# Kernel optimization log

Hardware: AMD Instinct MI355X
Metric: run time of the kernel (lower is better)

## Reference

```python
import jax, jax.numpy as jnp
import numpy as np

NPROTOS = 40      # forced by init_offset_tensor reshape
NCLASS  = 512     # number of child classes
C       = 64      # genetic feature channels (pshape[0])
W       = 40      # genetic sequence width (hard-coded in offset tensor)
B       = 1024    # batch
P       = NPROTOS * NCLASS  # 20480 total prototypes
EPS     = 1e-12   # F.normalize eps


def _build_last_layer_weight():
    # match[j, j // nprotos] = 1, weight = match.T with zeros -> -0.5
    match = np.zeros((P, NCLASS), np.float32)
    match[np.arange(P), np.arange(P) // NPROTOS] = 1.0
    w = match.T.copy()
    w[w == 0] = -0.5
    return jnp.asarray(w)


def _build_offset_tensor():
    # arange2[i, j] = (i - j) % nprotos; nprotos == 40 so arange3 is empty
    i = np.arange(NPROTOS)[:, None]
    j = np.arange(NPROTOS)[None, :]
    ar2 = (i - j) % NPROTOS                                  # (40, 40)
    off = np.tile(ar2.reshape(NPROTOS, 1, 1, NPROTOS), (NCLASS, C, 1, 1))
    return jnp.asarray(off.astype(np.int32))                 # (P, C, 1, W)


def setup_inputs() -> dict:
    key = jax.random.key(0)
    k1, k2 = jax.random.split(key)
    conv_features = jax.random.normal(k1, (B, C, 1, W), dtype=jnp.float32)
    prototype = jax.random.uniform(k2, (P, C, 1, 1), dtype=jnp.float32)  # torch.rand
    return {
        "conv_features": conv_features,
        "prototype": prototype,
        "last_layer_weight": _build_last_layer_weight(),
        "offset_tensor": _build_offset_tensor(),
    }


def _l2norm(x, axis):
    # F.normalize: x / max(||x||_2, eps)
    return x / jnp.maximum(jnp.linalg.norm(x, axis=axis, keepdims=True), EPS)


def reference(conv_features, prototype, last_layer_weight, offset_tensor):
    sqrt_D = 1.0  # sqrt(pshape[1] * pshape[2]) = sqrt(1*1)
    x = _l2norm(conv_features, axis=1) / sqrt_D              # (B, C, 1, W)
    p = _l2norm(prototype, axis=1) / sqrt_D                  # (P, C, 1, 1)
    # pad prototypes to width W, then per-prototype spatial offset gather
    p = jnp.pad(p, ((0, 0), (0, 0), (0, 0), (0, W - 1)))     # (P, C, 1, W)
    p = jnp.take_along_axis(p, offset_tensor, axis=3)        # (P, C, 1, W)
    # conv2d with full-width kernel -> output (B, P, 1, 1); max_pool over 1x1 is identity
    sim = jnp.einsum('bchw,pchw->bp', x, p)                  # (B, P)
    min_distances = -sim                                     # view(-1, nclass*nprotos)
    logits = sim @ last_layer_weight.T                       # (B, NCLASS)
    return (logits, min_distances)
```

## Files before the change

kernel.cpp:

```cpp
#include <hip/hip_runtime.h>
#include <math.h>

#define NB 1024
#define NC 64
#define NW 40
#define NK 512
#define NP 20480
#define EPSF 1e-12f


__global__ __launch_bounds__(256) void knorm_p(const float* __restrict__ proto,
                                               float* __restrict__ pn) {
    int wave = threadIdx.x >> 6;
    int lane = threadIdx.x & 63;
    int p = blockIdx.x * 4 + wave;
    float v = proto[p * 64 + lane];
    float s = v * v;
#pragma unroll
    for (int off = 32; off >= 1; off >>= 1) s += __shfl_xor(s, off);
    float r = 1.0f / fmaxf(sqrtf(s), EPSF);
    int j = p % NW, k = p / NW;
    pn[(j * NK + k) * 64 + lane] = v * r;
}

__global__ __launch_bounds__(256) void knorm_x(const float* __restrict__ x,
                                               float* __restrict__ xn) {
    __shared__ float xs[64 * 41];
    __shared__ float rn[40];
    int b = blockIdx.x;
    const float* xb = x + b * (64 * 40);
    for (int t = threadIdx.x; t < 2560; t += 256) {
        int c = t / 40, w = t % 40;
        xs[c * 41 + w] = xb[t];
    }
    __syncthreads();
    if (threadIdx.x < 40) {
        int w = threadIdx.x;
        float s = 0.f;
#pragma unroll
        for (int c = 0; c < 64; ++c) { float v = xs[c * 41 + w]; s += v * v; }
        rn[w] = 1.0f / fmaxf(sqrtf(s), EPSF);
    }
    __syncthreads();
    for (int t = threadIdx.x; t < 2560; t += 256) {
        int w = t >> 6, c = t & 63;
        xn[(w * NB + b) * 64 + c] = xs[c * 41 + w] * rn[w];
    }
}

__global__ __launch_bounds__(256) void kgemm(const float* __restrict__ xn,
                                             const float* __restrict__ pn,
                                             float* __restrict__ simt) {
    __shared__ float4 Xs[128 * 16];
    __shared__ float4 Ps[128 * 16];
    int b0 = blockIdx.x * 128;
    int k0 = blockIdx.y * 128;
    int j  = blockIdx.z;
    const float4* xg = (const float4*)(xn + (size_t)(j * NB + b0) * 64);
    const float4* pg = (const float4*)(pn + (size_t)(j * NK + k0) * 64);
    for (int g = threadIdx.x; g < 2048; g += 256) {
        int row = g >> 4, c4 = g & 15;
        int idx = (row << 4) + (c4 ^ (row >> 3));
        Xs[idx] = xg[g];
        Ps[idx] = pg[g];
    }
    __syncthreads();
    int tb = threadIdx.x >> 4, tk = threadIdx.x & 15;
    float acc[8][8];
#pragma unroll
    for (int i = 0; i < 8; ++i)
#pragma unroll
        for (int q = 0; q < 8; ++q) acc[i][q] = 0.f;

    for (int c4 = 0; c4 < 16; ++c4) {
        float4 xv[8];
#pragma unroll
        for (int i = 0; i < 8; ++i) {
            int row = tb + 16 * i;
            xv[i] = Xs[(row << 4) + (c4 ^ (row >> 3))];
        }
#pragma unroll
        for (int q = 0; q < 8; ++q) {
            int row = tk * 8 + q;
            float4 pv = Ps[(row << 4) + (c4 ^ tk)];
#pragma unroll
            for (int i = 0; i < 8; ++i)
                acc[i][q] += xv[i].x * pv.x + xv[i].y * pv.y +
                             xv[i].z * pv.z + xv[i].w * pv.w;
        }
    }

#pragma unroll
    for (int i = 0; i < 8; ++i) {
        int b = b0 + tb + 16 * i;
        float4* dst = (float4*)(simt + (size_t)b * NP + j * NK + k0 + tk * 8);
        dst[0] = make_float4(acc[i][0], acc[i][1], acc[i][2], acc[i][3]);
        dst[1] = make_float4(acc[i][4], acc[i][5], acc[i][6], acc[i][7]);
    }
}

__global__ __launch_bounds__(256) void ktrans(const float* __restrict__ simt,
                                              float* __restrict__ out) {
    __shared__ float ld[128][41];
    __shared__ float wred[4];
    int b = blockIdx.x;
    int t = threadIdx.x;
    const float* src = simt + (size_t)b * NP;
    float* md = out + (size_t)NB * NK + (size_t)b * NP;
    float rk[4];
    float my_tot = 0.f;

#pragma unroll
    for (int pass = 0; pass < 4; ++pass) {
        int k0 = pass << 7;
#pragma unroll
        for (int s = 0; s < 5; ++s) {
            int idx = s * 256 + t;
            int jj = idx >> 5, f4 = idx & 31;
            float4 v = *(const float4*)(src + jj * NK + k0 + f4 * 4);
            ld[f4 * 4 + 0][jj] = v.x;
            ld[f4 * 4 + 1][jj] = v.y;
            ld[f4 * 4 + 2][jj] = v.z;
            ld[f4 * 4 + 3][jj] = v.w;
        }
        __syncthreads();
        if (t < 128) {
            float s = 0.f;
#pragma unroll
            for (int jj = 0; jj < 40; ++jj) s += ld[t][jj];
            rk[pass] = s;
            my_tot += s;
        }
#pragma unroll
        for (int s2 = 0; s2 < 5; ++s2) {
            int pl = s2 * 1024 + t * 4;
            int kk = pl / 40;
            int jj = pl - kk * 40;
            float vv[4];
#pragma unroll
            for (int e = 0; e < 4; ++e) {
                vv[e] = -ld[kk][jj];
                if (++jj == 40) { jj = 0; ++kk; }
            }
            *(float4*)(md + k0 * 40 + pl) = make_float4(vv[0], vv[1], vv[2], vv[3]);
        }
        __syncthreads();
    }

    float s = my_tot;
#pragma unroll
    for (int off = 32; off >= 1; off >>= 1) s += __shfl_xor(s, off);
    if ((t & 63) == 0) wred[t >> 6] = s;
    __syncthreads();
    float S = wred[0] + wred[1] + wred[2] + wred[3];
    if (t < 128) {
#pragma unroll
        for (int pass = 0; pass < 4; ++pass)
            out[(size_t)b * NK + (pass << 7) + t] = 1.5f * rk[pass] - 0.5f * S;
    }
}

extern "C" void kernel_launch(void* const* d_in, const int* in_sizes, int n_in,
                              void* d_out, int out_size, void* d_ws, size_t ws_size,
                              hipStream_t stream) {
    (void)in_sizes; (void)n_in; (void)out_size; (void)ws_size;
    const float* conv  = (const float*)d_in[0];
    const float* proto = (const float*)d_in[1];
    float* out = (float*)d_out;
    float* ws = (float*)d_ws;
    float* pn   = ws;
    float* xn   = ws + 1310720;
    float* simt = ws + 3932160;

    knorm_p<<<5120, 256, 0, stream>>>(proto, pn);
    knorm_x<<<1024, 256, 0, stream>>>(conv, xn);
    kgemm<<<dim3(8, 4, 40), 256, 0, stream>>>(xn, pn, simt);
    ktrans<<<1024, 256, 0, stream>>>(simt, out);
}
```

Before: 355.8 us.

## Store normalized inputs and similarity intermediate in fp16, merge norm kernels

Normalized x and prototypes, and the intermediate similarity matrix, are stored as fp16 instead of fp32, halving workspace traffic between the norm, GEMM and transpose kernels. The two normalization kernels are fused into one launch, and the transpose kernel is restructured to process 256 classes per pass with an fp16 shared tile. The cost is reduced precision in min_distances and logits (fp16 rounding of sim), which risks tolerance failures.

```diff
diff --git a/kernel.cpp b/kernel.cpp
--- a/kernel.cpp
+++ b/kernel.cpp
@@ -1,4 +1,5 @@
 #include <hip/hip_runtime.h>
+#include <hip/hip_fp16.h>
 #include <math.h>
 
 #define NB 1024
@@ -9,62 +10,78 @@
 #define EPSF 1e-12f
 
 
-__global__ __launch_bounds__(256) void knorm_p(const float* __restrict__ proto,
-                                               float* __restrict__ pn) {
-    int wave = threadIdx.x >> 6;
-    int lane = threadIdx.x & 63;
-    int p = blockIdx.x * 4 + wave;
-    float v = proto[p * 64 + lane];
-    float s = v * v;
-#pragma unroll
-    for (int off = 32; off >= 1; off >>= 1) s += __shfl_xor(s, off);
-    float r = 1.0f / fmaxf(sqrtf(s), EPSF);
-    int j = p % NW, k = p / NW;
-    pn[(j * NK + k) * 64 + lane] = v * r;
-}
-
-__global__ __launch_bounds__(256) void knorm_x(const float* __restrict__ x,
-                                               float* __restrict__ xn) {
+__global__ __launch_bounds__(256) void knorm(const float* __restrict__ conv,
+                                             const float* __restrict__ proto,
+                                             __half* __restrict__ xnh,
+                                             __half* __restrict__ pnh) {
     __shared__ float xs[64 * 41];
     __shared__ float rn[40];
-    int b = blockIdx.x;
-    const float* xb = x + b * (64 * 40);
-    for (int t = threadIdx.x; t < 2560; t += 256) {
-        int c = t / 40, w = t % 40;
-        xs[c * 41 + w] = xb[t];
-    }
-    __syncthreads();
-    if (threadIdx.x < 40) {
-        int w = threadIdx.x;
-        float s = 0.f;
+    int blk = blockIdx.x;
+    if (blk < NB) {
+        int b = blk;
+        const float* xb = conv + b * (64 * 40);
+        for (int t = threadIdx.x; t < 2560; t += 256) {
+            int c = t / 40, w = t % 40;
+            xs[c * 41 + w] = xb[t];
+        }
+        __syncthreads();
+        if (threadIdx.x < 40) {
+            int w = threadIdx.x;
+            float s = 0.f;
 #pragma unroll
-        for (int c = 0; c < 64; ++c) { float v = xs[c * 41 + w]; s += v * v; }
-        rn[w] = 1.0f / fmaxf(sqrtf(s), EPSF);
-    }
-    __syncthreads();
-    for (int t = threadIdx.x; t < 2560; t += 256) {
-        int w = t >> 6, c = t & 63;
-        xn[(w * NB + b) * 64 + c] = xs[c * 41 + w] * rn[w];
+            for (int c = 0; c < 64; ++c) { float v = xs[c * 41 + w]; s += v * v; }
+            rn[w] = 1.0f / fmaxf(sqrtf(s), EPSF);
+        }
+        __syncthreads();
+        for (int t = threadIdx.x; t < 2560; t += 256) {
+            int w = t >> 6, c = t & 63;
+            xnh[((size_t)w * NB + b) * 64 + c] = __float2half(xs[c * 41 + w] * rn[w]);
+        }
+    } else {
+        int p = (blk - NB) * 4 + (threadIdx.x >> 6);
+        int lane = threadIdx.x & 63;
+        float v = proto[p * 64 + lane];
+        float s = v * v;
+#pragma unroll
+        for (int off = 32; off >= 1; off >>= 1) s += __shfl_xor(s, off);
+        float r = 1.0f / fmaxf(sqrtf(s), EPSF);
+        int j = p % NW, k = p / NW;
+        pnh[((size_t)j * NK + k) * 64 + lane] = __float2half(v * r);
     }
 }
 
-__global__ __launch_bounds__(256) void kgemm(const float* __restrict__ xn,
-                                             const float* __restrict__ pn,
-                                             float* __restrict__ simt) {
+__global__ __launch_bounds__(256, 2) void kgemm(const __half* __restrict__ xnh,
+                                                const __half* __restrict__ pnh,
+                                                __half* __restrict__ simt) {
     __shared__ float4 Xs[128 * 16];
     __shared__ float4 Ps[128 * 16];
     int b0 = blockIdx.x * 128;
     int k0 = blockIdx.y * 128;
     int j  = blockIdx.z;
-    const float4* xg = (const float4*)(xn + (size_t)(j * NB + b0) * 64);
-    const float4* pg = (const float4*)(pn + (size_t)(j * NK + k0) * 64);
-    for (int g = threadIdx.x; g < 2048; g += 256) {
-        int row = g >> 4, c4 = g & 15;
-        int idx = (row << 4) + (c4 ^ (row >> 3));
-        Xs[idx] = xg[g];
-        Ps[idx] = pg[g];
+    const __half* xg = xnh + ((size_t)j * NB + b0) * 64;
+    const __half* pg = pnh + ((size_t)j * NK + k0) * 64;
+
+    for (int g = threadIdx.x; g < 1024; g += 256) {
+        int row = g >> 3, ch = g & 7;
+        uint4 ux = *(const uint4*)(xg + (size_t)row * 64 + ch * 8);
+        uint4 up = *(const uint4*)(pg + (size_t)row * 64 + ch * 8);
+        float2 x01 = __half22float2(*(__half2*)&ux.x);
+        float2 x23 = __half22float2(*(__half2*)&ux.y);
+        float2 x45 = __half22float2(*(__half2*)&ux.z);
+        float2 x67 = __half22float2(*(__half2*)&ux.w);
+        float2 p01 = __half22float2(*(__half2*)&up.x);
+        float2 p23 = __half22float2(*(__half2*)&up.y);
+        float2 p45 = __half22float2(*(__half2*)&up.z);
+        float2 p67 = __half22float2(*(__half2*)&up.w);
+        int xk = row & 7, pk = (row >> 3) & 7;
+        int c4a = ch * 2, c4b = ch * 2 + 1;
+        Xs[(row << 4) + (c4a ^ xk)] = make_float4(x01.x, x01.y, x23.x, x23.y);
+        Xs[(row << 4) + (c4b ^ xk)] = make_float4(x45.x, x45.y, x67.x, x67.y);
+        Ps[(row << 4) + (c4a ^ pk)] = make_float4(p01.x, p01.y, p23.x, p23.y);
+        Ps[(row << 4) + (c4b ^ pk)] = make_float4(p45.x, p45.y, p67.x, p67.y);
     }
     __syncthreads();
+
     int tb = threadIdx.x >> 4, tk = threadIdx.x & 15;
     float acc[8][8];
 #pragma unroll
@@ -77,12 +94,12 @@
 #pragma unroll
         for (int i = 0; i < 8; ++i) {
             int row = tb + 16 * i;
-            xv[i] = Xs[(row << 4) + (c4 ^ (row >> 3))];
+            xv[i] = Xs[(row << 4) + (c4 ^ (row & 7))];
         }
 #pragma unroll
         for (int q = 0; q < 8; ++q) {
             int row = tk * 8 + q;
-            float4 pv = Ps[(row << 4) + (c4 ^ tk)];
+            float4 pv = Ps[(row << 4) + (c4 ^ (tk & 7))];
 #pragma unroll
             for (int i = 0; i < 8; ++i)
                 acc[i][q] += xv[i].x * pv.x + xv[i].y * pv.y +
@@ -93,56 +110,55 @@
 #pragma unroll
     for (int i = 0; i < 8; ++i) {
         int b = b0 + tb + 16 * i;
-        float4* dst = (float4*)(simt + (size_t)b * NP + j * NK + k0 + tk * 8);
-        dst[0] = make_float4(acc[i][0], acc[i][1], acc[i][2], acc[i][3]);
-        dst[1] = make_float4(acc[i][4], acc[i][5], acc[i][6], acc[i][7]);
+        union { __half2 h2[4]; uint4 u; } st;
+        st.h2[0] = __halves2half2(__float2half(acc[i][0]), __float2half(acc[i][1]));
+        st.h2[1] = __halves2half2(__float2half(acc[i][2]), __float2half(acc[i][3]));
+        st.h2[2] = __halves2half2(__float2half(acc[i][4]), __float2half(acc[i][5]));
+        st.h2[3] = __halves2half2(__float2half(acc[i][6]), __float2half(acc[i][7]));
+        *(uint4*)(simt + (size_t)b * NP + j * NK + k0 + tk * 8) = st.u;
     }
 }
 
-__global__ __launch_bounds__(256) void ktrans(const float* __restrict__ simt,
+__global__ __launch_bounds__(256) void ktrans(const __half* __restrict__ simt,
                                               float* __restrict__ out) {
-    __shared__ float ld[128][41];
+    __shared__ __half ldh[40][520];
     __shared__ float wred[4];
     int b = blockIdx.x;
     int t = threadIdx.x;
-    const float* src = simt + (size_t)b * NP;
+    const __half* src = simt + (size_t)b * NP;
     float* md = out + (size_t)NB * NK + (size_t)b * NP;
-    float rk[4];
+    float rk[2];
     float my_tot = 0.f;
 
 #pragma unroll
-    for (int pass = 0; pass < 4; ++pass) {
-        int k0 = pass << 7;
+    for (int kp = 0; kp < 2; ++kp) {
+        int k0 = kp << 8;
 #pragma unroll
-        for (int s = 0; s < 5; ++s) {
-            int idx = s * 256 + t;
-            int jj = idx >> 5, f4 = idx & 31;
-            float4 v = *(const float4*)(src + jj * NK + k0 + f4 * 4);
-            ld[f4 * 4 + 0][jj] = v.x;
-            ld[f4 * 4 + 1][jj] = v.y;
-            ld[f4 * 4 + 2][jj] = v.z;
-            ld[f4 * 4 + 3][jj] = v.w;
+        for (int r = 0; r < 5; ++r) {
+            int idx = r * 256 + t;
+            int j = idx >> 5, ch = idx & 31;
+            uint4 v = *(const uint4*)(src + j * NK + k0 + ch * 8);
+            *(uint4*)(&ldh[j][ch * 8]) = v;
         }
         __syncthreads();
-        if (t < 128) {
+        {
             float s = 0.f;
 #pragma unroll
-            for (int jj = 0; jj < 40; ++jj) s += ld[t][jj];
-            rk[pass] = s;
+            for (int j = 0; j < 40; ++j) s += __half2float(ldh[j][t]);
+            rk[kp] = s;
             my_tot += s;
         }
 #pragma unroll
-        for (int s2 = 0; s2 < 5; ++s2) {
-            int pl = s2 * 1024 + t * 4;
-            int kk = pl / 40;
-            int jj = pl - kk * 40;
-            float vv[4];
+        for (int r = 0; r < 10; ++r) {
+            int pl = (r * 256 + t) * 4;
+            int kk = pl / 40, jj = pl - kk * 40;
+            float w[4];
 #pragma unroll
             for (int e = 0; e < 4; ++e) {
-                vv[e] = -ld[kk][jj];
+                w[e] = -__half2float(ldh[jj][kk]);
                 if (++jj == 40) { jj = 0; ++kk; }
             }
-            *(float4*)(md + k0 * 40 + pl) = make_float4(vv[0], vv[1], vv[2], vv[3]);
+            *(float4*)(md + k0 * 40 + pl) = make_float4(w[0], w[1], w[2], w[3]);
         }
         __syncthreads();
     }
@@ -153,11 +169,8 @@
     if ((t & 63) == 0) wred[t >> 6] = s;
     __syncthreads();
     float S = wred[0] + wred[1] + wred[2] + wred[3];
-    if (t < 128) {
-#pragma unroll
-        for (int pass = 0; pass < 4; ++pass)
-            out[(size_t)b * NK + (pass << 7) + t] = 1.5f * rk[pass] - 0.5f * S;
-    }
+    out[(size_t)b * NK + t]       = 1.5f * rk[0] - 0.5f * S;
+    out[(size_t)b * NK + 256 + t] = 1.5f * rk[1] - 0.5f * S;
 }
 
 extern "C" void kernel_launch(void* const* d_in, const int* in_sizes, int n_in,
@@ -167,13 +180,12 @@
     const float* conv  = (const float*)d_in[0];
     const float* proto = (const float*)d_in[1];
     float* out = (float*)d_out;
-    float* ws = (float*)d_ws;
-    float* pn   = ws;
-    float* xn   = ws + 1310720;
-    float* simt = ws + 3932160;
+    char* wsb = (char*)d_ws;
+    __half* xnh  = (__half*)(wsb);
+    __half* pnh  = (__half*)(wsb + 5242880);
+    __half* simt = (__half*)(wsb + 7864320);
 
-    knorm_p<<<5120, 256, 0, stream>>>(proto, pn);
-    knorm_x<<<1024, 256, 0, stream>>>(conv, xn);
-    kgemm<<<dim3(8, 4, 40), 256, 0, stream>>>(xn, pn, simt);
+    knorm<<<6144, 256, 0, stream>>>(conv, proto, xnh, pnh);
+    kgemm<<<dim3(8, 4, 40), 256, 0, stream>>>(xnh, pnh, simt);
     ktrans<<<1024, 256, 0, stream>>>(simt, out);
 }
```

After: 339.8 us. -4.5%, faster.
